# Performance work log

Hardware: AMD Instinct MI355X
Metric: run time of the kernel (lower is better)

Reference implementation:

```python
import jax, jax.numpy as jnp
import numpy as np

CLAMP_MIN, CLAMP_MAX = -3.0, 3.0
RANK = 16


def setup_inputs() -> dict:
    key = jax.random.key(0)
    ks = jax.random.split(key, 8)
    B, N, D, H, R = 8, 4096, 1024, 256, RANK
    s = 0.02  # small weight std so clamp/exp are well-conditioned
    return {
        "query_emb": jax.random.normal(ks[0], (B, D), jnp.float32),
        "context_embs": jax.random.normal(ks[1], (B, N, D), jnp.float32),
        "W1": jax.random.normal(ks[2], (D, H), jnp.float32) * s,
        "b1": jnp.zeros((H,), jnp.float32),
        "Wd": jax.random.normal(ks[3], (H, D), jnp.float32) * s,
        "bd": jnp.zeros((D,), jnp.float32),
        "WL": jax.random.normal(ks[4], (H, D * R), jnp.float32) * s,
        "bL": jnp.zeros((D * R,), jnp.float32),
        "Wdel": jax.random.normal(ks[5], (H, D), jnp.float32) * s,
        "bdel": jnp.zeros((D,), jnp.float32),
        "Wa": jax.random.normal(ks[6], (H, D), jnp.float32) * s,
        "ba": jnp.zeros((D,), jnp.float32),
    }


def reference(query_emb, context_embs, W1, b1, Wd, bd, WL, bL, Wdel, bdel, Wa, ba):
    B, N, D = context_embs.shape
    R = RANK
    # Backbone: Linear + ReLU (assumed MLP backbone)
    h = jax.nn.relu(query_emb @ W1 + b1)                      # (B,H)
    # Parameter heads (SkewGaussian.forward)
    log_d = jnp.clip(h @ Wd + bd, CLAMP_MIN, CLAMP_MAX)       # (B,D)
    L = (h @ WL + bL).reshape(B, D, R) * 0.1                  # (B,D,R)
    delta = (h @ Wdel + bdel) * 0.1                           # (B,D)
    alpha = h @ Wa + ba                                       # (B,D)

    mu = query_emb + delta                                    # (B,D)
    diff = context_embs - mu[:, None, :]                      # (B,N,D)
    d_inv = jnp.exp(-log_d)                                   # (B,D)

    # Diagonal Mahalanobis term
    mahal_diag = jnp.einsum('bnd,bd->bn', diff * diff, d_inv) # (B,N)

    # Woodbury correction with small RxR system per batch
    DinvL = d_inv[:, :, None] * L                             # (B,D,R)
    M = jnp.eye(R, dtype=L.dtype)[None] + jnp.einsum('bdr,bds->brs', L, DinvL)  # (B,R,R)
    M_inv = jnp.linalg.inv(M)
    v = diff * d_inv[:, None, :]                              # (B,N,D)
    w = jnp.einsum('bdr,bnd->brn', L, v)                      # (B,R,N)
    correction = jnp.sum(w * jnp.einsum('brs,bsn->brn', M_inv, w), axis=1)  # (B,N)

    mahal = mahal_diag - correction
    log_det = jnp.sum(log_d, axis=-1, keepdims=True) + jnp.linalg.slogdet(M)[1][:, None]  # (B,1)
    symmetric_score = -0.5 * (mahal + log_det)                # (B,N)

    skew_input = jnp.einsum('bd,bnd->bn', alpha, diff)
    skew_score = jax.nn.log_sigmoid(skew_input)
    return symmetric_score + skew_score
```

## Files before the change

### kernel.cpp

```cpp
#include <hip/hip_runtime.h>
#include <math.h>

#define BB 8
#define NN 4096
#define DD 1024
#define HH 256
#define RR 16

#define WS_GT      0
#define WS_MU      131072
#define WS_DINV    139264
#define WS_ALPHA   147456
#define WS_LOGD    155648
#define WS_H       163840
#define WS_LOGDET  165888
#define WS_MINV    165904
#define WS_L       167952

__global__ __launch_bounds__(256) void ka1_h(
    const float* __restrict__ qe, const float* __restrict__ W1,
    const float* __restrict__ b1, float* __restrict__ ws)
{
    const int b = blockIdx.x;
    const int c = threadIdx.x;
    __shared__ float qe_s[DD];
    for (int i = c; i < DD; i += 256) qe_s[i] = qe[b * DD + i];
    __syncthreads();
    float a0 = 0.f, a1 = 0.f, a2 = 0.f, a3 = 0.f;
    for (int d = 0; d < DD; d += 4) {
        a0 = fmaf(qe_s[d + 0], W1[(d + 0) * HH + c], a0);
        a1 = fmaf(qe_s[d + 1], W1[(d + 1) * HH + c], a1);
        a2 = fmaf(qe_s[d + 2], W1[(d + 2) * HH + c], a2);
        a3 = fmaf(qe_s[d + 3], W1[(d + 3) * HH + c], a3);
    }
    ws[WS_H + b * HH + c] = fmaxf((a0 + a1) + (a2 + a3) + b1[c], 0.f);
}

__global__ __launch_bounds__(256) void ka2_heads(
    const float* __restrict__ qe,
    const float* __restrict__ Wd, const float* __restrict__ bd,
    const float* __restrict__ WL, const float* __restrict__ bL,
    const float* __restrict__ Wdel, const float* __restrict__ bdel,
    const float* __restrict__ Wa, const float* __restrict__ ba,
    float* __restrict__ ws)
{
    __shared__ float h_s[BB * HH];
    const int tid = threadIdx.x;
    for (int i = tid; i < BB * HH; i += 256) h_s[i] = ws[WS_H + i];
    __syncthreads();

    const int blk = blockIdx.x;
    int mode, c;
    const float* W; const float* bias;
    if (blk < 4)       { mode = 0; c = blk * 256 + tid;        W = Wd;   bias = bd;   }
    else if (blk < 8)  { mode = 1; c = (blk - 4) * 256 + tid;  W = Wdel; bias = bdel; }
    else if (blk < 12) { mode = 2; c = (blk - 8) * 256 + tid;  W = Wa;   bias = ba;   }
    else               { mode = 3; c = (blk - 12) * 256 + tid; W = WL;   bias = bL;   }
    const int ld = (mode == 3) ? (DD * RR) : DD;

    float acc[8];
    const float bc = bias[c];
    #pragma unroll
    for (int b = 0; b < 8; ++b) acc[b] = bc;

    #pragma unroll 4
    for (int r = 0; r < HH; ++r) {
        const float w = W[r * ld + c];
        #pragma unroll
        for (int b = 0; b < 8; ++b) acc[b] = fmaf(h_s[b * HH + r], w, acc[b]);
    }

    if (mode == 0) {
        #pragma unroll
        for (int b = 0; b < 8; ++b) {
            const float ldv = fminf(fmaxf(acc[b], -3.f), 3.f);
            ws[WS_LOGD + b * DD + c] = ldv;
            ws[WS_DINV + b * DD + c] = expf(-ldv);
        }
    } else if (mode == 1) {
        #pragma unroll
        for (int b = 0; b < 8; ++b)
            ws[WS_MU + b * DD + c] = qe[b * DD + c] + 0.1f * acc[b];
    } else if (mode == 2) {
        #pragma unroll
        for (int b = 0; b < 8; ++b) ws[WS_ALPHA + b * DD + c] = acc[b];
    } else {
        #pragma unroll
        for (int b = 0; b < 8; ++b) ws[WS_L + b * DD * RR + c] = 0.1f * acc[b];
    }
}

__global__ __launch_bounds__(256) void kg_gt(float* __restrict__ ws)
{
    const int idx = blockIdx.x * 256 + threadIdx.x;
    const int d = idx & (DD - 1);
    const int r = (idx >> 10) & (RR - 1);
    const int b = idx >> 14;
    ws[WS_GT + idx] = ws[WS_DINV + b * DD + d] * ws[WS_L + (b * DD + d) * RR + r];
}

__global__ __launch_bounds__(256) void kb_solve(float* __restrict__ ws)
{
    const int b = blockIdx.x;
    const int tid = threadIdx.x;

    __shared__ float Mpart[16 * 16 * 16];
    __shared__ float A[16][33];
    __shared__ float red_s[256];

    const float* Lp = ws + WS_L + (size_t)b * (DD * RR);
    const float* Gt = ws + WS_GT + (size_t)b * (RR * DD);

    float lsum = 0.f;
    for (int i = tid; i < DD; i += 256) lsum += ws[WS_LOGD + b * DD + i];
    red_s[tid] = lsum;
    __syncthreads();
    for (int s = 128; s > 0; s >>= 1) {
        if (tid < s) red_s[tid] += red_s[tid + s];
        __syncthreads();
    }
    const float logdsum = red_s[0];
    __syncthreads();

    {
        const int g = tid >> 4, u = tid & 15;
        float acc[16];
        #pragma unroll
        for (int s = 0; s < 16; ++s) acc[s] = 0.f;
        for (int d = u; d < DD; d += 16) {
            const float lg = Gt[g * DD + d];
            const float4* Lr = (const float4*)(Lp + d * 16);
            float4 l0 = Lr[0], l1 = Lr[1], l2 = Lr[2], l3 = Lr[3];
            const float lv[16] = {l0.x, l0.y, l0.z, l0.w, l1.x, l1.y, l1.z, l1.w,
                                  l2.x, l2.y, l2.z, l2.w, l3.x, l3.y, l3.z, l3.w};
            #pragma unroll
            for (int s = 0; s < 16; ++s) acc[s] = fmaf(lg, lv[s], acc[s]);
        }
        #pragma unroll
        for (int s = 0; s < 16; ++s) Mpart[g * 256 + s * 16 + u] = acc[s];
    }
    __syncthreads();

    const int i = tid >> 4, j = tid & 15;
    {
        float m = (i == j) ? 1.f : 0.f;
        #pragma unroll
        for (int u = 0; u < 16; ++u) m += Mpart[i * 256 + j * 16 + u];
        A[i][j] = m;
        A[i][j + 16] = (i == j) ? 1.f : 0.f;
    }
    __syncthreads();

    float logdetM = 0.f;
    for (int k = 0; k < 16; ++k) {
        const float piv = A[k][k];
        if (tid == 0) logdetM += logf(piv);
        __syncthreads();
        if (i == k) {
            const float rinv = 1.f / piv;
            A[i][j] *= rinv;
            A[i][j + 16] *= rinv;
        }
        __syncthreads();
        const float f = (i == k) ? 0.f : A[i][k];
        __syncthreads();
        if (i != k) {
            A[i][j]      = fmaf(-f, A[k][j],      A[i][j]);
            A[i][j + 16] = fmaf(-f, A[k][j + 16], A[i][j + 16]);
        }
        __syncthreads();
    }

    ws[WS_MINV + b * 256 + i * 16 + j] = A[i][j + 16];
    if (tid == 0) ws[WS_LOGDET + b] = logdsum + logdetM;
}

__global__ __launch_bounds__(256, 2) void kc_main(
    const float* __restrict__ ctx, const float* __restrict__ ws, float* __restrict__ out)
{
    const int bid = blockIdx.x;
    const int b = bid >> 8;
    const int tile = bid & 255;
    const int wave = threadIdx.x >> 6;
    const int lane = threadIdx.x & 63;
    const int n0 = tile * 16 + wave * 4;

    const float4* Gt4 = (const float4*)(ws + WS_GT + (size_t)b * (RR * DD));
    const float4* mu4 = (const float4*)(ws + WS_MU + b * DD);
    const float4* dv4 = (const float4*)(ws + WS_DINV + b * DD);
    const float4* al4 = (const float4*)(ws + WS_ALPHA + b * DD);
    const float4* ctx4 = (const float4*)(ctx + ((size_t)(b * NN + n0)) * DD);

    float g[4][16];
    float md[4], aa[4];
    #pragma unroll
    for (int i = 0; i < 4; ++i) {
        md[i] = 0.f; aa[i] = 0.f;
        #pragma unroll
        for (int r = 0; r < 16; ++r) g[i][r] = 0.f;
    }

    #pragma unroll
    for (int step = 0; step < 4; ++step) {
        const int fi = step * 64 + lane;
        const float4 mv = mu4[fi], dvv = dv4[fi], av = al4[fi];
        const float4 c0 = ctx4[0 * (DD / 4) + fi];
        const float4 c1 = ctx4[1 * (DD / 4) + fi];
        const float4 c2 = ctx4[2 * (DD / 4) + fi];
        const float4 c3 = ctx4[3 * (DD / 4) + fi];

        float diff[4][4];
        diff[0][0] = c0.x - mv.x; diff[0][1] = c0.y - mv.y; diff[0][2] = c0.z - mv.z; diff[0][3] = c0.w - mv.w;
        diff[1][0] = c1.x - mv.x; diff[1][1] = c1.y - mv.y; diff[1][2] = c1.z - mv.z; diff[1][3] = c1.w - mv.w;
        diff[2][0] = c2.x - mv.x; diff[2][1] = c2.y - mv.y; diff[2][2] = c2.z - mv.z; diff[2][3] = c2.w - mv.w;
        diff[3][0] = c3.x - mv.x; diff[3][1] = c3.y - mv.y; diff[3][2] = c3.z - mv.z; diff[3][3] = c3.w - mv.w;

        const float dva[4] = {dvv.x, dvv.y, dvv.z, dvv.w};
        const float ava[4] = {av.x, av.y, av.z, av.w};
        #pragma unroll
        for (int i = 0; i < 4; ++i) {
            #pragma unroll
            for (int j = 0; j < 4; ++j) {
                md[i] = fmaf(diff[i][j] * dva[j], diff[i][j], md[i]);
                aa[i] = fmaf(ava[j], diff[i][j], aa[i]);
            }
        }

        #pragma unroll
        for (int r = 0; r < 16; ++r) {
            const float4 gt = Gt4[r * 256 + fi];
            #pragma unroll
            for (int i = 0; i < 4; ++i) {
                g[i][r] = fmaf(gt.x, diff[i][0], g[i][r]);
                g[i][r] = fmaf(gt.y, diff[i][1], g[i][r]);
                g[i][r] = fmaf(gt.z, diff[i][2], g[i][r]);
                g[i][r] = fmaf(gt.w, diff[i][3], g[i][r]);
            }
        }
    }

    float v[64];
    #pragma unroll
    for (int i = 0; i < 4; ++i)
        #pragma unroll
        for (int r = 0; r < 16; ++r) v[i * 16 + r] = g[i][r];

    #pragma unroll
    for (int s6 = 0; s6 < 6; ++s6) {
        const int m = 1 << s6;
        const int half = 32 >> s6;
        const bool up = (lane & m) != 0;
        #pragma unroll
        for (int ii = 0; ii < half; ++ii) {
            float x0 = v[2 * ii], x1 = v[2 * ii + 1];
            float y0 = __shfl_xor(x0, m, 64);
            float y1 = __shfl_xor(x1, m, 64);
            v[ii] = up ? (x1 + y1) : (x0 + y0);
        }
    }
    const float w = v[0];

    #pragma unroll
    for (int m = 1; m < 64; m <<= 1) {
        #pragma unroll
        for (int i = 0; i < 4; ++i) {
            md[i] += __shfl_xor(md[i], m, 64);
            aa[i] += __shfl_xor(aa[i], m, 64);
        }
    }

    const int r = lane & 15;
    const int rowbase = lane & 48;
    const float* Minv = ws + WS_MINV + b * 256 + r * 16;
    float y = 0.f;
    #pragma unroll
    for (int s = 0; s < 16; ++s) y = fmaf(Minv[s], __shfl(w, rowbase + s, 64), y);
    float corr = w * y;
    corr += __shfl_xor(corr, 1, 64);
    corr += __shfl_xor(corr, 2, 64);
    corr += __shfl_xor(corr, 4, 64);
    corr += __shfl_xor(corr, 8, 64);

    const float ld = ws[WS_LOGDET + b];
    if ((lane & 15) == 0) {
        const int i = lane >> 4;
        const float mdv = (i & 2) ? ((i & 1) ? md[3] : md[2]) : ((i & 1) ? md[1] : md[0]);
        const float aav = (i & 2) ? ((i & 1) ? aa[3] : aa[2]) : ((i & 1) ? aa[1] : aa[0]);
        const float lsig = fminf(aav, 0.f) - log1pf(expf(-fabsf(aav)));
        out[(size_t)b * NN + n0 + i] = -0.5f * (mdv - corr + ld) + lsig;
    }
}

extern "C" void kernel_launch(void* const* d_in, const int* in_sizes, int n_in,
                              void* d_out, int out_size, void* d_ws, size_t ws_size,
                              hipStream_t stream)
{
    const float* qe   = (const float*)d_in[0];
    const float* ctx  = (const float*)d_in[1];
    const float* W1   = (const float*)d_in[2];
    const float* b1   = (const float*)d_in[3];
    const float* Wd   = (const float*)d_in[4];
    const float* bd   = (const float*)d_in[5];
    const float* WL   = (const float*)d_in[6];
    const float* bL   = (const float*)d_in[7];
    const float* Wdel = (const float*)d_in[8];
    const float* bdel = (const float*)d_in[9];
    const float* Wa   = (const float*)d_in[10];
    const float* ba   = (const float*)d_in[11];
    float* out = (float*)d_out;
    float* ws  = (float*)d_ws;

    ka1_h<<<8, 256, 0, stream>>>(qe, W1, b1, ws);
    ka2_heads<<<76, 256, 0, stream>>>(qe, Wd, bd, WL, bL, Wdel, bdel, Wa, ba, ws);
    kg_gt<<<512, 256, 0, stream>>>(ws);
    kb_solve<<<8, 256, 0, stream>>>(ws);
    kc_main<<<2048, 256, 0, stream>>>(ctx, ws, out);
}
```

Measured before the change: 348.0 us.

## Split small prologue kernels for more parallelism and stage Gt in LDS

```diff
diff --git a/kernel.cpp b/kernel.cpp
--- a/kernel.cpp
+++ b/kernel.cpp
@@ -11,33 +11,35 @@
 #define WS_MU      131072
 #define WS_DINV    139264
 #define WS_ALPHA   147456
-#define WS_LOGD    155648
-#define WS_H       163840
-#define WS_LOGDET  165888
-#define WS_MINV    165904
-#define WS_L       167952
+#define WS_HP      155648
+#define WS_LDP     163840
+#define WS_M       163968
+#define WS_MINV    166016
+#define WS_LOGDET  168064
+#define WS_L       168080
 
 __global__ __launch_bounds__(256) void ka1_h(
-    const float* __restrict__ qe, const float* __restrict__ W1,
-    const float* __restrict__ b1, float* __restrict__ ws)
-{
-    const int b = blockIdx.x;
+    const float* __restrict__ qe, const float* __restrict__ W1, float* __restrict__ ws)
+{
+    const int b = blockIdx.x >> 2;
+    const int sl = blockIdx.x & 3;
     const int c = threadIdx.x;
-    __shared__ float qe_s[DD];
-    for (int i = c; i < DD; i += 256) qe_s[i] = qe[b * DD + i];
+    __shared__ float qe_s[256];
+    qe_s[c] = qe[b * DD + sl * 256 + c];
     __syncthreads();
     float a0 = 0.f, a1 = 0.f, a2 = 0.f, a3 = 0.f;
-    for (int d = 0; d < DD; d += 4) {
-        a0 = fmaf(qe_s[d + 0], W1[(d + 0) * HH + c], a0);
-        a1 = fmaf(qe_s[d + 1], W1[(d + 1) * HH + c], a1);
-        a2 = fmaf(qe_s[d + 2], W1[(d + 2) * HH + c], a2);
-        a3 = fmaf(qe_s[d + 3], W1[(d + 3) * HH + c], a3);
-    }
-    ws[WS_H + b * HH + c] = fmaxf((a0 + a1) + (a2 + a3) + b1[c], 0.f);
+    const float* W1p = W1 + (sl * 256) * HH;
+    for (int dl = 0; dl < 256; dl += 4) {
+        a0 = fmaf(qe_s[dl + 0], W1p[(dl + 0) * HH + c], a0);
+        a1 = fmaf(qe_s[dl + 1], W1p[(dl + 1) * HH + c], a1);
+        a2 = fmaf(qe_s[dl + 2], W1p[(dl + 2) * HH + c], a2);
+        a3 = fmaf(qe_s[dl + 3], W1p[(dl + 3) * HH + c], a3);
+    }
+    ws[WS_HP + (b * 4 + sl) * HH + c] = (a0 + a1) + (a2 + a3);
 }
 
 __global__ __launch_bounds__(256) void ka2_heads(
-    const float* __restrict__ qe,
+    const float* __restrict__ qe, const float* __restrict__ b1,
     const float* __restrict__ Wd, const float* __restrict__ bd,
     const float* __restrict__ WL, const float* __restrict__ bL,
     const float* __restrict__ Wdel, const float* __restrict__ bdel,
@@ -45,48 +47,68 @@
     float* __restrict__ ws)
 {
     __shared__ float h_s[BB * HH];
+    __shared__ float red[4][512];
     const int tid = threadIdx.x;
-    for (int i = tid; i < BB * HH; i += 256) h_s[i] = ws[WS_H + i];
+
+    for (int i = tid; i < BB * HH; i += 256) {
+        const int bb = i >> 8, c = i & 255;
+        const float v = ws[WS_HP + (bb * 4 + 0) * HH + c] + ws[WS_HP + (bb * 4 + 1) * HH + c]
+                      + ws[WS_HP + (bb * 4 + 2) * HH + c] + ws[WS_HP + (bb * 4 + 3) * HH + c]
+                      + b1[c];
+        h_s[i] = fmaxf(v, 0.f);
+    }
     __syncthreads();
 
     const int blk = blockIdx.x;
-    int mode, c;
-    const float* W; const float* bias;
-    if (blk < 4)       { mode = 0; c = blk * 256 + tid;        W = Wd;   bias = bd;   }
-    else if (blk < 8)  { mode = 1; c = (blk - 4) * 256 + tid;  W = Wdel; bias = bdel; }
-    else if (blk < 12) { mode = 2; c = (blk - 8) * 256 + tid;  W = Wa;   bias = ba;   }
-    else               { mode = 3; c = (blk - 12) * 256 + tid; W = WL;   bias = bL;   }
+    const int lane = tid & 63;
+    const int u = tid >> 6;
+
+    int mode; const float* W; const float* bias; int base;
+    if (blk < 16)       { mode = 0; W = Wd;   bias = bd;   base = 0;  }
+    else if (blk < 32)  { mode = 1; W = Wdel; bias = bdel; base = 16; }
+    else if (blk < 48)  { mode = 2; W = Wa;   bias = ba;   base = 32; }
+    else                { mode = 3; W = WL;   bias = bL;   base = 48; }
     const int ld = (mode == 3) ? (DD * RR) : DD;
+    const int cc = (blk - base) * 64 + lane;
 
     float acc[8];
-    const float bc = bias[c];
-    #pragma unroll
-    for (int b = 0; b < 8; ++b) acc[b] = bc;
+    #pragma unroll
+    for (int b = 0; b < 8; ++b) acc[b] = 0.f;
 
     #pragma unroll 4
-    for (int r = 0; r < HH; ++r) {
-        const float w = W[r * ld + c];
-        #pragma unroll
-        for (int b = 0; b < 8; ++b) acc[b] = fmaf(h_s[b * HH + r], w, acc[b]);
-    }
-
+    for (int rr = 0; rr < 64; ++rr) {
+        const int r = u * 64 + rr;
+        const float wv = W[r * ld + cc];
+        #pragma unroll
+        for (int b = 0; b < 8; ++b) acc[b] = fmaf(h_s[b * HH + r], wv, acc[b]);
+    }
+    #pragma unroll
+    for (int b = 0; b < 8; ++b) red[u][lane * 8 + b] = acc[b];
+    __syncthreads();
+
+    for (int e = tid; e < 512; e += 256) {
+        const int cl = e >> 3, bb = e & 7;
+        const int cm = (blk - base) * 64 + cl;
+        float s = red[0][e] + red[1][e] + red[2][e] + red[3][e] + bias[cm];
+        if (mode == 0) {
+            const float ldv = fminf(fmaxf(s, -3.f), 3.f);
+            ws[WS_DINV + bb * DD + cm] = expf(-ldv);
+            red[0][e] = ldv;
+        } else if (mode == 1) {
+            ws[WS_MU + bb * DD + cm] = qe[bb * DD + cm] + 0.1f * s;
+        } else if (mode == 2) {
+            ws[WS_ALPHA + bb * DD + cm] = s;
+        } else {
+            ws[WS_L + bb * (DD * RR) + cm] = 0.1f * s;
+        }
+    }
     if (mode == 0) {
-        #pragma unroll
-        for (int b = 0; b < 8; ++b) {
-            const float ldv = fminf(fmaxf(acc[b], -3.f), 3.f);
-            ws[WS_LOGD + b * DD + c] = ldv;
-            ws[WS_DINV + b * DD + c] = expf(-ldv);
-        }
-    } else if (mode == 1) {
-        #pragma unroll
-        for (int b = 0; b < 8; ++b)
-            ws[WS_MU + b * DD + c] = qe[b * DD + c] + 0.1f * acc[b];
-    } else if (mode == 2) {
-        #pragma unroll
-        for (int b = 0; b < 8; ++b) ws[WS_ALPHA + b * DD + c] = acc[b];
-    } else {
-        #pragma unroll
-        for (int b = 0; b < 8; ++b) ws[WS_L + b * DD * RR + c] = 0.1f * acc[b];
+        __syncthreads();
+        if (tid < 8) {
+            float s = 0.f;
+            for (int cl = 0; cl < 64; ++cl) s += red[0][cl * 8 + tid];
+            ws[WS_LDP + blk * 8 + tid] = s;
+        }
     }
 }
 
@@ -99,56 +121,42 @@
     ws[WS_GT + idx] = ws[WS_DINV + b * DD + d] * ws[WS_L + (b * DD + d) * RR + r];
 }
 
-__global__ __launch_bounds__(256) void kb_solve(float* __restrict__ ws)
+__global__ __launch_bounds__(256) void kM(float* __restrict__ ws)
+{
+    const int b = blockIdx.x >> 4;
+    const int g = blockIdx.x & 15;
+    const int tid = threadIdx.x;
+    const int s = tid & 15, dg = tid >> 4;
+
+    const float* Gt = ws + WS_GT + (size_t)b * (RR * DD) + g * DD;
+    const float* Lp = ws + WS_L + (size_t)b * (DD * RR);
+
+    float acc = 0.f;
+    #pragma unroll 4
+    for (int k = 0; k < 64; ++k) {
+        const int d = dg * 64 + k;
+        acc = fmaf(Gt[d], Lp[d * 16 + s], acc);
+    }
+    __shared__ float red2[16][17];
+    red2[dg][s] = acc;
+    __syncthreads();
+    if (tid < 16) {
+        float m = (tid == g) ? 1.f : 0.f;
+        #pragma unroll
+        for (int d2 = 0; d2 < 16; ++d2) m += red2[d2][tid];
+        ws[WS_M + b * 256 + g * 16 + tid] = m;
+    }
+}
+
+__global__ __launch_bounds__(256) void kGJ(float* __restrict__ ws)
 {
     const int b = blockIdx.x;
     const int tid = threadIdx.x;
-
-    __shared__ float Mpart[16 * 16 * 16];
+    const int i = tid >> 4, j = tid & 15;
     __shared__ float A[16][33];
-    __shared__ float red_s[256];
-
-    const float* Lp = ws + WS_L + (size_t)b * (DD * RR);
-    const float* Gt = ws + WS_GT + (size_t)b * (RR * DD);
-
-    float lsum = 0.f;
-    for (int i = tid; i < DD; i += 256) lsum += ws[WS_LOGD + b * DD + i];
-    red_s[tid] = lsum;
-    __syncthreads();
-    for (int s = 128; s > 0; s >>= 1) {
-        if (tid < s) red_s[tid] += red_s[tid + s];
-        __syncthreads();
-    }
-    const float logdsum = red_s[0];
-    __syncthreads();
-
-    {
-        const int g = tid >> 4, u = tid & 15;
-        float acc[16];
-        #pragma unroll
-        for (int s = 0; s < 16; ++s) acc[s] = 0.f;
-        for (int d = u; d < DD; d += 16) {
-            const float lg = Gt[g * DD + d];
-            const float4* Lr = (const float4*)(Lp + d * 16);
-            float4 l0 = Lr[0], l1 = Lr[1], l2 = Lr[2], l3 = Lr[3];
-            const float lv[16] = {l0.x, l0.y, l0.z, l0.w, l1.x, l1.y, l1.z, l1.w,
-                                  l2.x, l2.y, l2.z, l2.w, l3.x, l3.y, l3.z, l3.w};
-            #pragma unroll
-            for (int s = 0; s < 16; ++s) acc[s] = fmaf(lg, lv[s], acc[s]);
-        }
-        #pragma unroll
-        for (int s = 0; s < 16; ++s) Mpart[g * 256 + s * 16 + u] = acc[s];
-    }
-    __syncthreads();
-
-    const int i = tid >> 4, j = tid & 15;
-    {
-        float m = (i == j) ? 1.f : 0.f;
-        #pragma unroll
-        for (int u = 0; u < 16; ++u) m += Mpart[i * 256 + j * 16 + u];
-        A[i][j] = m;
-        A[i][j + 16] = (i == j) ? 1.f : 0.f;
-    }
+
+    A[i][j] = ws[WS_M + b * 256 + i * 16 + j];
+    A[i][j + 16] = (i == j) ? 1.f : 0.f;
     __syncthreads();
 
     float logdetM = 0.f;
@@ -170,22 +178,33 @@
         }
         __syncthreads();
     }
-
     ws[WS_MINV + b * 256 + i * 16 + j] = A[i][j + 16];
-    if (tid == 0) ws[WS_LOGDET + b] = logdsum + logdetM;
-}
-
-__global__ __launch_bounds__(256, 2) void kc_main(
+    if (tid == 0) {
+        float lds = 0.f;
+        for (int k = 0; k < 16; ++k) lds += ws[WS_LDP + k * 8 + b];
+        ws[WS_LOGDET + b] = lds + logdetM;
+    }
+}
+
+__global__ __launch_bounds__(512, 4) void kc_main(
     const float* __restrict__ ctx, const float* __restrict__ ws, float* __restrict__ out)
 {
     const int bid = blockIdx.x;
-    const int b = bid >> 8;
-    const int tile = bid & 255;
+    const int b = bid >> 7;
+    const int tile = bid & 127;
     const int wave = threadIdx.x >> 6;
     const int lane = threadIdx.x & 63;
-    const int n0 = tile * 16 + wave * 4;
-
-    const float4* Gt4 = (const float4*)(ws + WS_GT + (size_t)b * (RR * DD));
+    const int n0 = tile * 32 + wave * 4;
+
+    __shared__ float gt_s[RR * DD];
+    {
+        float4* gs4 = (float4*)gt_s;
+        const float4* Gt4g = (const float4*)(ws + WS_GT + (size_t)b * (RR * DD));
+        for (int i = threadIdx.x; i < RR * DD / 4; i += 512) gs4[i] = Gt4g[i];
+    }
+    __syncthreads();
+    const float4* gs4 = (const float4*)gt_s;
+
     const float4* mu4 = (const float4*)(ws + WS_MU + b * DD);
     const float4* dv4 = (const float4*)(ws + WS_DINV + b * DD);
     const float4* al4 = (const float4*)(ws + WS_ALPHA + b * DD);
@@ -228,7 +247,7 @@
 
         #pragma unroll
         for (int r = 0; r < 16; ++r) {
-            const float4 gt = Gt4[r * 256 + fi];
+            const float4 gt = gs4[r * 256 + fi];
             #pragma unroll
             for (int i = 0; i < 4; ++i) {
                 g[i][r] = fmaf(gt.x, diff[i][0], g[i][r]);
@@ -310,9 +329,10 @@
     float* out = (float*)d_out;
     float* ws  = (float*)d_ws;
 
-    ka1_h<<<8, 256, 0, stream>>>(qe, W1, b1, ws);
-    ka2_heads<<<76, 256, 0, stream>>>(qe, Wd, bd, WL, bL, Wdel, bdel, Wa, ba, ws);
+    ka1_h<<<32, 256, 0, stream>>>(qe, W1, ws);
+    ka2_heads<<<304, 256, 0, stream>>>(qe, b1, Wd, bd, WL, bL, Wdel, bdel, Wa, ba, ws);
     kg_gt<<<512, 256, 0, stream>>>(ws);
-    kb_solve<<<8, 256, 0, stream>>>(ws);
-    kc_main<<<2048, 256, 0, stream>>>(ctx, ws, out);
-}
+    kM<<<128, 256, 0, stream>>>(ws);
+    kGJ<<<8, 256, 0, stream>>>(ws);
+    kc_main<<<1024, 512, 0, stream>>>(ctx, ws, out);
+}
```

After: 326.2 us. 6.3% less time.
